# Performance work log

Measured on AMD Instinct MI355X. Metric: run time of the kernel, lower is better.

Reference implementation:

```python
import jax, jax.numpy as jnp
import numpy as np

HEADS = 8
DIM_HEAD = 64
SCALE = DIM_HEAD ** -0.5
QUERY_DIM = 512
CTX_DIM = 64
INNER = HEADS * DIM_HEAD  # 512
GATE_HID = 32


def setup_inputs() -> dict:
    key = jax.random.key(0)
    ks = jax.random.split(key, 11)
    B, N, M = 4, 2048, 2048
    s = lambda fan: 1.0 / np.sqrt(fan)
    return {
        "x": jax.random.normal(ks[0], (B, N, QUERY_DIM), dtype=jnp.float32),
        "context": jax.random.normal(ks[1], (B, M, CTX_DIM), dtype=jnp.float32),
        "Wq": jax.random.normal(ks[2], (QUERY_DIM, INNER), dtype=jnp.float32) * s(QUERY_DIM),
        "Wk": jax.random.normal(ks[3], (CTX_DIM, INNER), dtype=jnp.float32) * s(CTX_DIM),
        "Wv": jax.random.normal(ks[4], (CTX_DIM, INNER), dtype=jnp.float32) * s(CTX_DIM),
        "W1": jax.random.normal(ks[5], (CTX_DIM, GATE_HID), dtype=jnp.float32) * s(CTX_DIM),
        "b1": jnp.zeros((GATE_HID,), dtype=jnp.float32),
        "W2": jax.random.normal(ks[6], (GATE_HID, 1), dtype=jnp.float32) * s(GATE_HID),
        "b2": jnp.zeros((1,), dtype=jnp.float32),
        "Wo": jax.random.normal(ks[7], (INNER, QUERY_DIM), dtype=jnp.float32) * s(INNER),
        "bo": jnp.zeros((QUERY_DIM,), dtype=jnp.float32),
    }


def reference(x, context, Wq, Wk, Wv, W1, b1, W2, b2, Wo, bo):
    B, N, _ = x.shape
    M = context.shape[1]
    # visual reliability gate: sigmoid(relu(ctx @ W1 + b1) @ W2 + b2) -> [B, M, 1]
    gate = jax.nn.sigmoid(jax.nn.relu(context @ W1 + b1) @ W2 + b2)
    ctx = context * gate
    # projections
    q = (x @ Wq).reshape(B, N, HEADS, DIM_HEAD).transpose(0, 2, 1, 3)    # [B,H,N,D]
    k = (ctx @ Wk).reshape(B, M, HEADS, DIM_HEAD).transpose(0, 2, 1, 3)  # [B,H,M,D]
    v = (ctx @ Wv).reshape(B, M, HEADS, DIM_HEAD).transpose(0, 2, 1, 3)  # [B,H,M,D]
    # scaled dot-product attention (full score matrix, as in source)
    sim = jnp.einsum('bhid,bhjd->bhij', q, k) * SCALE
    attn = jax.nn.softmax(sim, axis=-1)
    out = jnp.einsum('bhij,bhjd->bhid', attn, v)
    out = out.transpose(0, 2, 1, 3).reshape(B, N, INNER)
    return out @ Wo + bo
```

## Files before the change

kernel.cpp:

```cpp
#include <hip/hip_runtime.h>

typedef unsigned short u16;
typedef unsigned int u32;
using frag16 = __attribute__((ext_vector_type(8))) short;
using facc   = __attribute__((ext_vector_type(4))) float;
using facc16 = __attribute__((ext_vector_type(16))) float;

#define DEV static __device__ __forceinline__

DEV u16 f2bf(float f) {
  union { float f; unsigned u; } v; v.f = f;
  unsigned r = v.u + 0x7fffu + ((v.u >> 16) & 1u);
  return (u16)(r >> 16);
}
DEV unsigned fbits(float f) {
  union { float f; unsigned u; } v; v.f = f;
  return v.u;
}
DEV unsigned pkbf(float lo, float hi) {
  return __builtin_amdgcn_perm(fbits(hi) + 0x8000u, fbits(lo) + 0x8000u, 0x07060302u);
}
DEV void gld16(const u16* g, u16* l) {
  __builtin_amdgcn_global_load_lds(
      (__attribute__((address_space(1))) unsigned int*)(g),
      (__attribute__((address_space(3))) unsigned int*)(l), 16, 0, 0);
}

__global__ __launch_bounds__(256) void prep_gate_kernel(const float4* __restrict__ x,
    const float* __restrict__ Wq, const float* __restrict__ Wk,
    const float* __restrict__ Wv, const float* __restrict__ Wo,
    const float* __restrict__ ctx, const float* __restrict__ W1,
    const float* __restrict__ b1, const float* __restrict__ W2,
    const float* __restrict__ b2,
    u16* __restrict__ xb, u16* __restrict__ WqT, u16* __restrict__ WkT,
    u16* __restrict__ WvT, u16* __restrict__ WoT, u16* __restrict__ gctx) {
  int bid = blockIdx.x;
  if (bid < 4096) {
    int id = bid * 256 + threadIdx.x;
    float4 v = x[id];
    ushort4 o;
    o.x = f2bf(v.x); o.y = f2bf(v.y); o.z = f2bf(v.z); o.w = f2bf(v.w);
    *(ushort4*)(xb + (size_t)id * 4) = o;
  } else if (bid < 6400) {
    int id = (bid - 4096) * 256 + threadIdx.x;
    const float* W; u16* WT; int K, idx;
    if (id < 262144)      { W = Wq; WT = WqT; K = 512; idx = id; }
    else if (id < 294912) { W = Wk; WT = WkT; K = 64;  idx = id - 262144; }
    else if (id < 327680) { W = Wv; WT = WvT; K = 64;  idx = id - 294912; }
    else                  { W = Wo; WT = WoT; K = 512; idx = id - 327680; }
    int n = idx / K, k = idx - n * K;
    WT[idx] = f2bf(W[k * 512 + n]);
  } else {
    int wave = threadIdx.x >> 6, lane = threadIdx.x & 63;
    int row = (bid - 6400) * 4 + wave;
    __shared__ float sc[4][64];
    float cv = ctx[(size_t)row * 64 + lane];
    sc[wave][lane] = cv;
    __syncthreads();
    float h = 0.f;
    if (lane < 32) {
      h = b1[lane];
      #pragma unroll
      for (int i = 0; i < 64; ++i) h += sc[wave][i] * W1[i * 32 + lane];
      h = fmaxf(h, 0.f) * W2[lane];
    }
    #pragma unroll
    for (int off = 32; off; off >>= 1) h += __shfl_xor(h, off);
    float g = 1.f / (1.f + __expf(-(h + b2[0])));
    gctx[(size_t)row * 64 + lane] = f2bf(cv * g);
  }
}

template<int MODE>
DEV void gemm128_body(const u16* __restrict__ A, const u16* __restrict__ BT,
                      void* __restrict__ Cp, const float* __restrict__ bias,
                      int m0, int n0, float scale,
                      u16* As0, u16* As1, u16* Bs0, u16* Bs1) {
  const int K = 512, N = 512;
  const int lane = threadIdx.x & 63, wave = threadIdx.x >> 6;
  const int quad = lane >> 4, l16 = lane & 15;
  const int wr = wave >> 1, wc = wave & 1;

  const u16* gA = A + (size_t)(m0 + wave * 32 + (lane >> 2)) * K + (lane & 3) * 8;
  const u16* gB = BT + (size_t)(n0 + wave * 16 + (lane >> 2)) * K + (lane & 3) * 8;

  facc acc[4][2] = {};

  for (int k0 = 0; k0 < K; k0 += 64) {
    if (k0) __syncthreads();
    gld16(gA + k0,           As0 + wave * 1024);
    gld16(gA + 16 * K + k0,  As0 + wave * 1024 + 512);
    gld16(gA + k0 + 32,          As1 + wave * 1024);
    gld16(gA + 16 * K + k0 + 32, As1 + wave * 1024 + 512);
    gld16(gB + k0,      Bs0 + wave * 512);
    gld16(gB + k0 + 32, Bs1 + wave * 512);
    __syncthreads();

    #pragma unroll
    for (int hh = 0; hh < 2; ++hh) {
      const u16* Ah = hh ? As1 : As0;
      const u16* Bh = hh ? Bs1 : Bs0;
      frag16 af[4], bf[2];
      #pragma unroll
      for (int rt = 0; rt < 4; ++rt)
        af[rt] = *(const frag16*)(Ah + (wr * 64 + rt * 16 + l16) * 32 + quad * 8);
      #pragma unroll
      for (int ct = 0; ct < 2; ++ct)
        bf[ct] = *(const frag16*)(Bh + (wc * 32 + ct * 16 + l16) * 32 + quad * 8);
      #pragma unroll
      for (int rt = 0; rt < 4; ++rt)
        #pragma unroll
        for (int ct = 0; ct < 2; ++ct)
          acc[rt][ct] = __builtin_amdgcn_mfma_f32_16x16x32_bf16(af[rt], bf[ct], acc[rt][ct], 0, 0, 0);
    }
  }

  #pragma unroll
  for (int rt = 0; rt < 4; ++rt) {
    #pragma unroll
    for (int ct = 0; ct < 2; ++ct) {
      int col = n0 + wc * 32 + ct * 16 + l16;
      int r0g = m0 + wr * 64 + rt * 16 + quad * 4;
      if (MODE == 0) {
        u16* C = (u16*)Cp;
        #pragma unroll
        for (int r = 0; r < 4; ++r)
          C[(size_t)(r0g + r) * N + col] = f2bf(acc[rt][ct][r] * scale);
      } else {
        float* C = (float*)Cp;
        float bv = bias[col];
        #pragma unroll
        for (int r = 0; r < 4; ++r)
          C[(size_t)(r0g + r) * N + col] = acc[rt][ct][r] + bv;
      }
    }
  }
}

__global__ __launch_bounds__(256) void proj_kernel(const u16* __restrict__ xb,
    const u16* __restrict__ WqT, u16* __restrict__ qb,
    const u16* __restrict__ gctx, const u16* __restrict__ BkT,
    const u16* __restrict__ BvT, u16* __restrict__ Kp, u16* __restrict__ Vp) {
  __shared__ __align__(16) u16 As0[128 * 32], As1[128 * 32];
  __shared__ __align__(16) u16 Bs0[64 * 32], Bs1[64 * 32];
  int bid = blockIdx.x;
  if (bid < 512) {
    int n0 = (bid & 7) * 64, m0 = (bid >> 3) * 128;
    gemm128_body<0>(xb, WqT, qb, nullptr, m0, n0,
                    0.125f * 1.4426950408889634f, As0, As1, Bs0, Bs1);
    return;
  }
  bid -= 512;
  const int Kd = 64;
  int lane = threadIdx.x & 63, wave = threadIdx.x >> 6;
  int quad = lane >> 4, l16 = lane & 15;
  int wr = wave >> 1, wc = wave & 1;
  int rowBase = (bid >> 3) * 64 + wr * 32;
  int colBase = (bid & 7) * 64 + wc * 32;
  facc ak[2][2] = {}, av[2][2] = {};
  const u16* a0 = gctx + (size_t)(rowBase + l16) * Kd + quad * 8;
  const u16* a1 = a0 + (size_t)16 * Kd;
  const u16* bk0 = BkT + (size_t)(colBase + l16) * Kd + quad * 8;
  const u16* bk1 = bk0 + (size_t)16 * Kd;
  const u16* bv0 = BvT + (size_t)(colBase + l16) * Kd + quad * 8;
  const u16* bv1 = bv0 + (size_t)16 * Kd;
  #pragma unroll
  for (int kk = 0; kk < Kd; kk += 32) {
    frag16 af0 = *(const frag16*)(a0 + kk);
    frag16 af1 = *(const frag16*)(a1 + kk);
    frag16 k0 = *(const frag16*)(bk0 + kk);
    frag16 k1 = *(const frag16*)(bk1 + kk);
    frag16 v0 = *(const frag16*)(bv0 + kk);
    frag16 v1 = *(const frag16*)(bv1 + kk);
    ak[0][0] = __builtin_amdgcn_mfma_f32_16x16x32_bf16(af0, k0, ak[0][0], 0, 0, 0);
    ak[0][1] = __builtin_amdgcn_mfma_f32_16x16x32_bf16(af0, k1, ak[0][1], 0, 0, 0);
    ak[1][0] = __builtin_amdgcn_mfma_f32_16x16x32_bf16(af1, k0, ak[1][0], 0, 0, 0);
    ak[1][1] = __builtin_amdgcn_mfma_f32_16x16x32_bf16(af1, k1, ak[1][1], 0, 0, 0);
    av[0][0] = __builtin_amdgcn_mfma_f32_16x16x32_bf16(af0, v0, av[0][0], 0, 0, 0);
    av[0][1] = __builtin_amdgcn_mfma_f32_16x16x32_bf16(af0, v1, av[0][1], 0, 0, 0);
    av[1][0] = __builtin_amdgcn_mfma_f32_16x16x32_bf16(af1, v0, av[1][0], 0, 0, 0);
    av[1][1] = __builtin_amdgcn_mfma_f32_16x16x32_bf16(af1, v1, av[1][1], 0, 0, 0);
  }
  #pragma unroll
  for (int rt = 0; rt < 2; ++rt) {
    #pragma unroll
    for (int ct = 0; ct < 2; ++ct) {
      int col = colBase + ct * 16 + l16;
      int r0g = rowBase + rt * 16 + quad * 4;
      int hh = col >> 6, d = col & 63;
      int b = r0g >> 11;
      #pragma unroll
      for (int r = 0; r < 4; ++r) {
        int m = (r0g + r) & 2047;
        size_t addr = ((((size_t)(b * 8 + hh) * 64 + (m >> 5)) * 4 + (d >> 4)) * 64
                       + ((d >> 3) & 1) * 32 + (m & 31)) * 8 + (d & 7);
        Kp[addr] = f2bf(ak[rt][ct][r]);
      }
      int m = r0g & 2047;
      size_t addr = ((((size_t)(b * 8 + hh) * 64 + (m >> 5)) * 4
                      + ((m >> 4) & 1) * 2 + (d >> 5)) * 64
                     + ((m >> 3) & 1) * 32 + (d & 31)) * 8 + (m & 7);
      ushort4 o;
      o.x = f2bf(av[rt][ct][0]); o.y = f2bf(av[rt][ct][1]);
      o.z = f2bf(av[rt][ct][2]); o.w = f2bf(av[rt][ct][3]);
      *(ushort4*)(Vp + addr) = o;
    }
  }
}

__global__ __launch_bounds__(256, 3) void attn_kernel(
    const u16* __restrict__ qb, const u16* __restrict__ Kp,
    const u16* __restrict__ Vp, float* __restrict__ Opart,
    float* __restrict__ Lpart) {
  const int lane = threadIdx.x & 63, wave = threadIdx.x >> 6;
  const int l32 = lane & 31;
  const int hi = lane >> 5;
  const int bid = blockIdx.x;
  const int bh = bid & 31;
  const int qblk = (bid >> 5) & 15;
  const int js = bid >> 9;
  const int b = bh >> 3, h = bh & 7;
  const int q0 = (qblk * 4 + wave) * 32;
  const int rowg = b * 2048 + q0 + l32;

  const u16* qp = qb + (size_t)rowg * 512 + h * 64 + hi * 8;
  frag16 qf0 = *(const frag16*)(qp);
  frag16 qf1 = *(const frag16*)(qp + 16);
  frag16 qf2 = *(const frag16*)(qp + 32);
  frag16 qf3 = *(const frag16*)(qp + 48);

  facc16 O0 = {}, O1 = {};
  float lsum = 0.f;

  const size_t ts = 2048;
  const u16* kpb = Kp + (size_t)(bh * 64 + js * 32) * ts + lane * 8;
  const u16* vpb = Vp + (size_t)(bh * 64 + js * 32) * ts + lane * 8;

  frag16 kA[4], vA[4], kB[4], vB[4];
  #pragma unroll
  for (int i = 0; i < 4; ++i) {
    kA[i] = *(const frag16*)(kpb + i * 512);
    vA[i] = *(const frag16*)(vpb + i * 512);
    kB[i] = *(const frag16*)(kpb + ts + i * 512);
    vB[i] = *(const frag16*)(vpb + ts + i * 512);
  }

  auto computeTile = [&](frag16* kf, frag16* vf) {
    facc16 S = {};
    S = __builtin_amdgcn_mfma_f32_32x32x16_bf16(kf[0], qf0, S, 0, 0, 0);
    S = __builtin_amdgcn_mfma_f32_32x32x16_bf16(kf[1], qf1, S, 0, 0, 0);
    S = __builtin_amdgcn_mfma_f32_32x32x16_bf16(kf[2], qf2, S, 0, 0, 0);
    S = __builtin_amdgcn_mfma_f32_32x32x16_bf16(kf[3], qf3, S, 0, 0, 0);
    float e[16];
    #pragma unroll
    for (int r = 0; r < 16; ++r) e[r] = __builtin_amdgcn_exp2f(S[r]);
    #pragma unroll
    for (int r = 0; r < 16; ++r) lsum += e[r];
    unsigned pu[2][4];
    #pragma unroll
    for (int c = 0; c < 2; ++c) {
      const float* ee = e + c * 8;
      unsigned L0 = pkbf(ee[0], ee[1]);
      unsigned L1 = pkbf(ee[2], ee[3]);
      unsigned H0 = pkbf(ee[4], ee[5]);
      unsigned H1 = pkbf(ee[6], ee[7]);
      unsigned Y0 = hi ? L0 : H0;
      unsigned Y1 = hi ? L1 : H1;
      unsigned X0 = (unsigned)__shfl_xor((int)Y0, 32);
      unsigned X1 = (unsigned)__shfl_xor((int)Y1, 32);
      pu[c][0] = hi ? X0 : L0;
      pu[c][1] = hi ? X1 : L1;
      pu[c][2] = hi ? H0 : X0;
      pu[c][3] = hi ? H1 : X1;
    }
    frag16 P0 = *(frag16*)&pu[0][0];
    frag16 P1 = *(frag16*)&pu[1][0];
    O0 = __builtin_amdgcn_mfma_f32_32x32x16_bf16(vf[0], P0, O0, 0, 0, 0);
    O0 = __builtin_amdgcn_mfma_f32_32x32x16_bf16(vf[2], P1, O0, 0, 0, 0);
    O1 = __builtin_amdgcn_mfma_f32_32x32x16_bf16(vf[1], P0, O1, 0, 0, 0);
    O1 = __builtin_amdgcn_mfma_f32_32x32x16_bf16(vf[3], P1, O1, 0, 0, 0);
  };

  for (int t = 0; t < 32; t += 2) {
    computeTile(kA, vA);
    {
      int tn = (t + 2 < 32) ? t + 2 : 31;
      const u16* kt = kpb + (size_t)tn * ts;
      const u16* vt = vpb + (size_t)tn * ts;
      #pragma unroll
      for (int i = 0; i < 4; ++i) {
        kA[i] = *(const frag16*)(kt + i * 512);
        vA[i] = *(const frag16*)(vt + i * 512);
      }
    }
    computeTile(kB, vB);
    {
      int tn = (t + 3 < 32) ? t + 3 : 31;
      const u16* kt = kpb + (size_t)tn * ts;
      const u16* vt = vpb + (size_t)tn * ts;
      #pragma unroll
      for (int i = 0; i < 4; ++i) {
        kB[i] = *(const frag16*)(kt + i * 512);
        vB[i] = *(const frag16*)(vt + i * 512);
      }
    }
  }

  lsum += __shfl_xor(lsum, 32);

  float* op = Opart + ((size_t)js * 8192 + rowg) * 512 + h * 64;
  #pragma unroll
  for (int dt = 0; dt < 2; ++dt) {
    #pragma unroll
    for (int rq = 0; rq < 4; ++rq) {
      float4 v;
      if (dt == 0) { v.x = O0[rq*4]; v.y = O0[rq*4+1]; v.z = O0[rq*4+2]; v.w = O0[rq*4+3]; }
      else         { v.x = O1[rq*4]; v.y = O1[rq*4+1]; v.z = O1[rq*4+2]; v.w = O1[rq*4+3]; }
      int d0 = dt * 32 + 8 * rq + 4 * hi;
      *(float4*)(op + d0) = v;
    }
  }
  if (!hi) Lpart[(size_t)js * 65536 + (size_t)rowg * 8 + h] = lsum;
}

__global__ __launch_bounds__(256) void combine_kernel(const float* __restrict__ Opart,
    const float* __restrict__ Lpart, u16* __restrict__ ob) {
  int id = blockIdx.x * 256 + threadIdx.x;
  int row = id >> 7, c4 = (id & 127) * 4;
  int hh = c4 >> 6;
  size_t o = (size_t)row * 512 + c4;
  const float4 o0 = *(const float4*)(Opart + o);
  const float4 o1 = *(const float4*)(Opart + (size_t)8192 * 512 + o);
  float rl = 1.f / (Lpart[(size_t)row * 8 + hh] + Lpart[65536 + (size_t)row * 8 + hh]);
  ushort4 u;
  u.x = f2bf((o0.x + o1.x) * rl);
  u.y = f2bf((o0.y + o1.y) * rl);
  u.z = f2bf((o0.z + o1.z) * rl);
  u.w = f2bf((o0.w + o1.w) * rl);
  *(ushort4*)(ob + o) = u;
}

__global__ __launch_bounds__(256) void gemm_out(const u16* __restrict__ A,
    const u16* __restrict__ BT, float* __restrict__ C,
    const float* __restrict__ bias) {
  __shared__ __align__(16) u16 As0[128 * 32], As1[128 * 32];
  __shared__ __align__(16) u16 Bs0[64 * 32], Bs1[64 * 32];
  int n0 = (blockIdx.x & 7) * 64, m0 = (blockIdx.x >> 3) * 128;
  gemm128_body<2>(A, BT, C, bias, m0, n0, 1.f, As0, As1, Bs0, Bs1);
}

extern "C" void kernel_launch(void* const* d_in, const int* in_sizes, int n_in,
                              void* d_out, int out_size, void* d_ws, size_t ws_size,
                              hipStream_t stream) {
  const float* x   = (const float*)d_in[0];
  const float* ctx = (const float*)d_in[1];
  const float* Wq  = (const float*)d_in[2];
  const float* Wk  = (const float*)d_in[3];
  const float* Wv  = (const float*)d_in[4];
  const float* W1  = (const float*)d_in[5];
  const float* b1  = (const float*)d_in[6];
  const float* W2  = (const float*)d_in[7];
  const float* b2  = (const float*)d_in[8];
  const float* Wo  = (const float*)d_in[9];
  const float* bo  = (const float*)d_in[10];
  float* out = (float*)d_out;

  char* ws = (char*)d_ws;
  size_t off = 0;
  auto alloc = [&](size_t bytes) {
    char* p = ws + off;
    off += (bytes + 255) & ~(size_t)255;
    return p;
  };
  u16* xb    = (u16*)alloc(8192ull * 512 * 2);
  u16* qb    = (u16*)alloc(8192ull * 512 * 2);
  u16* Kp    = (u16*)alloc(8192ull * 512 * 2);
  u16* Vp    = (u16*)alloc(8192ull * 512 * 2);
  u16* ob    = (u16*)alloc(8192ull * 512 * 2);
  u16* gctx  = (u16*)alloc(8192ull * 64 * 2);
  u16* WqT   = (u16*)alloc(512ull * 512 * 2);
  u16* WkT   = (u16*)alloc(512ull * 64 * 2);
  u16* WvT   = (u16*)alloc(512ull * 64 * 2);
  u16* WoT   = (u16*)alloc(512ull * 512 * 2);
  float* Opart = (float*)alloc(2ull * 8192 * 512 * 4);
  float* Lpart = (float*)alloc(2ull * 65536 * 4);

  prep_gate_kernel<<<8448, 256, 0, stream>>>((const float4*)x, Wq, Wk, Wv, Wo,
                                             ctx, W1, b1, W2, b2,
                                             xb, WqT, WkT, WvT, WoT, gctx);
  proj_kernel<<<1536, 256, 0, stream>>>(xb, WqT, qb, gctx, WkT, WvT, Kp, Vp);
  attn_kernel<<<1024, 256, 0, stream>>>(qb, Kp, Vp, Opart, Lpart);
  combine_kernel<<<4096, 256, 0, stream>>>(Opart, Lpart, ob);
  gemm_out<<<512, 256, 0, stream>>>(ob, WoT, out, bo);
}
```

Baseline: 187.3 us.

## Stage K/V tiles through double-buffered LDS shared across waves

```diff
diff --git a/kernel.cpp b/kernel.cpp
--- a/kernel.cpp
+++ b/kernel.cpp
@@ -223,6 +223,8 @@
   const int q0 = (qblk * 4 + wave) * 32;
   const int rowg = b * 2048 + q0 + l32;
 
+  __shared__ __align__(16) u16 sK[2][2048], sV[2][2048];
+
   const u16* qp = qb + (size_t)rowg * 512 + h * 64 + hi * 8;
   frag16 qf0 = *(const frag16*)(qp);
   frag16 qf1 = *(const frag16*)(qp + 16);
@@ -233,29 +235,39 @@
   float lsum = 0.f;
 
   const size_t ts = 2048;
-  const u16* kpb = Kp + (size_t)(bh * 64 + js * 32) * ts + lane * 8;
-  const u16* vpb = Vp + (size_t)(bh * 64 + js * 32) * ts + lane * 8;
-
-  frag16 kA[4], vA[4], kB[4], vB[4];
-  #pragma unroll
-  for (int i = 0; i < 4; ++i) {
-    kA[i] = *(const frag16*)(kpb + i * 512);
-    vA[i] = *(const frag16*)(vpb + i * 512);
-    kB[i] = *(const frag16*)(kpb + ts + i * 512);
-    vB[i] = *(const frag16*)(vpb + ts + i * 512);
-  }
-
-  auto computeTile = [&](frag16* kf, frag16* vf) {
+  const u16* kpb = Kp + (size_t)(bh * 64 + js * 32) * ts + wave * 512 + lane * 8;
+  const u16* vpb = Vp + (size_t)(bh * 64 + js * 32) * ts + wave * 512 + lane * 8;
+
+  gld16(kpb, sK[0] + wave * 512);
+  gld16(vpb, sV[0] + wave * 512);
+
+  for (int t = 0; t < 32; ++t) {
+    const int p = t & 1;
+    __syncthreads();
+    if (t + 1 < 32) {
+      gld16(kpb + (size_t)(t + 1) * ts, sK[p ^ 1] + wave * 512);
+      gld16(vpb + (size_t)(t + 1) * ts, sV[p ^ 1] + wave * 512);
+    }
+
+    frag16 kf[4], vf[4];
+    #pragma unroll
+    for (int i = 0; i < 4; ++i) {
+      kf[i] = *(const frag16*)(sK[p] + i * 512 + lane * 8);
+      vf[i] = *(const frag16*)(sV[p] + i * 512 + lane * 8);
+    }
+
     facc16 S = {};
     S = __builtin_amdgcn_mfma_f32_32x32x16_bf16(kf[0], qf0, S, 0, 0, 0);
     S = __builtin_amdgcn_mfma_f32_32x32x16_bf16(kf[1], qf1, S, 0, 0, 0);
     S = __builtin_amdgcn_mfma_f32_32x32x16_bf16(kf[2], qf2, S, 0, 0, 0);
     S = __builtin_amdgcn_mfma_f32_32x32x16_bf16(kf[3], qf3, S, 0, 0, 0);
+
     float e[16];
     #pragma unroll
     for (int r = 0; r < 16; ++r) e[r] = __builtin_amdgcn_exp2f(S[r]);
     #pragma unroll
     for (int r = 0; r < 16; ++r) lsum += e[r];
+
     unsigned pu[2][4];
     #pragma unroll
     for (int c = 0; c < 2; ++c) {
@@ -275,35 +287,11 @@
     }
     frag16 P0 = *(frag16*)&pu[0][0];
     frag16 P1 = *(frag16*)&pu[1][0];
+
     O0 = __builtin_amdgcn_mfma_f32_32x32x16_bf16(vf[0], P0, O0, 0, 0, 0);
     O0 = __builtin_amdgcn_mfma_f32_32x32x16_bf16(vf[2], P1, O0, 0, 0, 0);
     O1 = __builtin_amdgcn_mfma_f32_32x32x16_bf16(vf[1], P0, O1, 0, 0, 0);
     O1 = __builtin_amdgcn_mfma_f32_32x32x16_bf16(vf[3], P1, O1, 0, 0, 0);
-  };
-
-  for (int t = 0; t < 32; t += 2) {
-    computeTile(kA, vA);
-    {
-      int tn = (t + 2 < 32) ? t + 2 : 31;
-      const u16* kt = kpb + (size_t)tn * ts;
-      const u16* vt = vpb + (size_t)tn * ts;
-      #pragma unroll
-      for (int i = 0; i < 4; ++i) {
-        kA[i] = *(const frag16*)(kt + i * 512);
-        vA[i] = *(const frag16*)(vt + i * 512);
-      }
-    }
-    computeTile(kB, vB);
-    {
-      int tn = (t + 3 < 32) ? t + 3 : 31;
-      const u16* kt = kpb + (size_t)tn * ts;
-      const u16* vt = vpb + (size_t)tn * ts;
-      #pragma unroll
-      for (int i = 0; i < 4; ++i) {
-        kB[i] = *(const frag16*)(kt + i * 512);
-        vB[i] = *(const frag16*)(vt + i * 512);
-      }
-    }
   }
 
   lsum += __shfl_xor(lsum, 32);
```

Measured after the change: 181.6 us. 3.1% less time.
